# Performance work log

Measured on AMD Instinct MI355X. Metric: run time of the kernel, lower is better.

## Reference

```python
import jax, jax.numpy as jnp
import numpy as np
import math

SEQ = 45000
FEAT = 30
DEPTH, HEADS, DK, MLP, C = 4, 4, 32, 512, 32
MAXSEQ = 512


def pos_embed_table():
    # Enformer-style basis functions over distances [-SEQ+1, SEQ-1]
    d = jnp.arange(-SEQ + 1, SEQ, dtype=jnp.float32)
    a = jnp.abs(d)[:, None]
    nb = FEAT // 6  # basis per class (exponential / central-mask / gamma)
    # exponential decay
    hl = 2.0 ** jnp.linspace(3.0, math.log(SEQ) / math.log(2.0), nb)
    e1 = jnp.exp(-math.log(2.0) / hl[None, :] * a)
    # central mask
    cw = 2.0 ** jnp.arange(1, nb + 1, dtype=jnp.float32) - 1.0
    e2 = (cw[None, :] > a).astype(jnp.float32)
    # gamma pdf
    stddev = SEQ / (2 * nb)
    start_mean = SEQ / nb
    mean = jnp.linspace(start_mean, float(SEQ), nb)
    conc = (mean / stddev) ** 2
    rate = mean / stddev ** 2
    logp = jax.scipy.special.xlogy(conc - 1.0, a) - rate * a
    logz = jax.scipy.special.gammaln(conc) - conc * jnp.log(rate)
    p = jnp.exp(logp - logz) + 1e-8
    e3 = p / jnp.max(p)
    e = jnp.concatenate([e1, e2, e3], axis=-1)
    return jnp.concatenate([e, jnp.sign(d)[:, None] * e], axis=-1)  # [2*SEQ-1, FEAT]


def layernorm(x, g, b, eps=1e-5):
    mu = jnp.mean(x, axis=-1, keepdims=True)
    var = jnp.var(x, axis=-1, keepdims=True)
    return (x - mu) * jax.lax.rsqrt(var + eps) * g + b


def setup_inputs() -> dict:
    key = jax.random.key(0)
    ks = jax.random.split(key, 16)
    B, L = 2, SEQ
    HD = HEADS * DK
    s = 0.02
    return {
        "x_skip": jax.random.normal(ks[0], (B, C, L), jnp.float32),
        "attention": jax.random.uniform(ks[1], (B, 3, L), jnp.float32),
        "ln1_g": jnp.ones((DEPTH, C), jnp.float32),
        "ln1_b": jnp.zeros((DEPTH, C), jnp.float32),
        "Wq": jax.random.normal(ks[2], (DEPTH, C, HD), jnp.float32) * s,
        "Wk": jax.random.normal(ks[3], (DEPTH, C, HD), jnp.float32) * s,
        "Wv": jax.random.normal(ks[4], (DEPTH, C, HD), jnp.float32) * s,
        "Wrel": jax.random.normal(ks[5], (DEPTH, FEAT, HD), jnp.float32) * s,
        "rcb": jax.random.normal(ks[6], (DEPTH, HEADS, DK), jnp.float32),
        "rpb": jax.random.normal(ks[7], (DEPTH, HEADS, DK), jnp.float32),
        "Wo": jax.random.normal(ks[8], (DEPTH, HD, C), jnp.float32) * s,
        "bo": jnp.zeros((DEPTH, C), jnp.float32),
        "ln2_g": jnp.ones((DEPTH, C), jnp.float32),
        "ln2_b": jnp.zeros((DEPTH, C), jnp.float32),
        "W1": jax.random.normal(ks[9], (DEPTH, C, MLP), jnp.float32) * s,
        "b1": jnp.zeros((DEPTH, MLP), jnp.float32),
        "W2": jax.random.normal(ks[10], (DEPTH, MLP, C), jnp.float32) * s,
        "b2": jnp.zeros((DEPTH, C), jnp.float32),
    }


def reference(x_skip, attention, ln1_g, ln1_b, Wq, Wk, Wv, Wrel, rcb, rpb, Wo, bo, ln2_g, ln2_b, W1, b1, W2, b2):
    B, Cc, L = x_skip.shape
    half = MAXSEQ // 2
    x_emb = jnp.swapaxes(x_skip, 1, 2)  # [B, L, C]
    # top splice sites by acceptor / donor score
    acc = jnp.argsort(-attention[:, 1, :], axis=1)[:, :half]
    don = jnp.argsort(-attention[:, 2, :], axis=1)[:, :half]
    idx = jnp.sort(jnp.concatenate([acc, don], axis=1), axis=1)  # [B, n]
    n = idx.shape[1]
    diff = idx[:, :, None] - idx[:, None, :] + SEQ - 1  # [B, n, n]
    positions = pos_embed_table()[diff]  # [B, n, n, FEAT]
    emb = jnp.take_along_axis(x_emb, idx[:, :, None], axis=1)  # [B, n, C]
    scale = DK ** -0.5
    for l in range(DEPTH):
        h = layernorm(emb, ln1_g[l], ln1_b[l])
        q = (h @ Wq[l]).reshape(B, n, HEADS, DK).transpose(0, 2, 1, 3) * scale
        k = (h @ Wk[l]).reshape(B, n, HEADS, DK).transpose(0, 2, 1, 3)
        v = (h @ Wv[l]).reshape(B, n, HEADS, DK).transpose(0, 2, 1, 3)
        content = jnp.einsum('bhid,bhjd->bhij', q + rcb[l][None, :, None, :], k)
        rel_k = (positions @ Wrel[l]).reshape(B, n, n, HEADS, DK)  # b i j h d
        rel = jnp.einsum('bhid,bijhd->bhij', q + rpb[l][None, :, None, :], rel_k)
        attn_w = jax.nn.softmax(content + rel, axis=-1)
        o = jnp.einsum('bhij,bhjd->bhid', attn_w, v)
        o = o.transpose(0, 2, 1, 3).reshape(B, n, HEADS * DK)
        emb = emb + o @ Wo[l] + bo[l]
        h2 = layernorm(emb, ln2_g[l], ln2_b[l])
        emb = emb + jax.nn.gelu(h2 @ W1[l] + b1[l], approximate=False) @ W2[l] + b2[l]
    out = jnp.zeros_like(x_emb).at[jnp.arange(B)[:, None], idx].set(emb)
    return jnp.swapaxes(out, 1, 2)  # [B, C, L]
```

## Files before the change

kernel.cpp:

```cpp
#include <hip/hip_runtime.h>
#include <math.h>

#define SEQL   45000
#define NBAT   2
#define CCH    32
#define NSEL   512
#define NHEAD  4
#define DKD    32
#define HDD    128
#define MLPD   512
#define CDCAP  2048
#define TKB    32
#define ETB    176

__device__ __forceinline__ unsigned short f2bf(float x) {
  unsigned u = __float_as_uint(x);
  u = (u + 0x7fffu + ((u >> 16) & 1u)) >> 16;
  return (unsigned short)u;
}
#define BFL(u) __uint_as_float((u) << 16)
#define BFH(u) __uint_as_float((u) & 0xffff0000u)

__global__ __launch_bounds__(256) void prep_kernel(const float* __restrict__ att,
                                                   unsigned char* __restrict__ E16,
                                                   int* __restrict__ hist,
                                                   float* __restrict__ out) {
  {
    int nthr = gridDim.x * 256;
    int gt = blockIdx.x * 256 + threadIdx.x;
    float4 z4 = make_float4(0.f, 0.f, 0.f, 0.f);
    float4* o4 = (float4*)out;
    for (int i = gt; i < NBAT * CCH * SEQL / 4; i += nthr) o4[i] = z4;
  }
  if (blockIdx.x < ETB) {
    int a = blockIdx.x * 256 + threadIdx.x;
    if (a >= SEQL) return;
    float ad = (float)a;
    float outv[16];
    float log2S = log2f((float)SEQL);
    #pragma unroll
    for (int k = 0; k < 5; ++k) {
      float hl = exp2f(3.0f + (float)k * (log2S - 3.0f) * 0.25f);
      outv[k] = exp2f(-ad / hl);
    }
    const int cw[5] = {1, 3, 7, 15, 31};
    #pragma unroll
    for (int k = 0; k < 5; ++k) outv[5 + k] = (a < cw[k]) ? 1.0f : 0.0f;
    float pmax = 0.0f;
    float pk[5];
    #pragma unroll
    for (int k = 0; k < 5; ++k) {
      float mean = 9000.0f * (float)(k + 1);
      float sd = 4500.0f;
      float cc = (mean / sd) * (mean / sd);
      float rr = mean / (sd * sd);
      float logz = lgammaf(cc) - cc * logf(rr);
      float pp;
      if (a == 0) pp = 1e-8f;
      else pp = expf((cc - 1.0f) * logf(ad) - rr * ad - logz) + 1e-8f;
      pk[k] = pp;
      float mstar = (cc - 1.0f) / rr;
      float m0 = floorf(mstar), m1 = m0 + 1.0f;
      if (m1 > (float)(SEQL - 1)) m1 = (float)(SEQL - 1);
      float p0 = expf((cc - 1.0f) * logf(m0) - rr * m0 - logz) + 1e-8f;
      float p1 = expf((cc - 1.0f) * logf(m1) - rr * m1 - logz) + 1e-8f;
      pmax = fmaxf(pmax, fmaxf(p0, p1));
    }
    #pragma unroll
    for (int k = 0; k < 5; ++k) outv[10 + k] = pk[k] / pmax;
    outv[15] = 0.0f;
    unsigned by[16];
    #pragma unroll
    for (int k = 0; k < 15; ++k)
      by[k] = (unsigned)(fminf(fmaxf(outv[k], 0.f), 1.f) * 255.f + 0.5f);
    by[15] = 0u;
    unsigned pw[8];
    #pragma unroll
    for (int k = 0; k < 8; ++k)
      pw[k] = (unsigned)f2bf((float)by[2 * k]) |
              ((unsigned)f2bf((float)by[2 * k + 1]) << 16);
    uint4 o0 = make_uint4(pw[0], pw[1], pw[2], pw[3]);
    uint4 o1 = make_uint4(pw[4], pw[5], pw[6], pw[7]);
    uint4* dst = (uint4*)(E16 + (size_t)a * 32);
    dst[0] = o0;
    dst[1] = o1;
  } else {
    int bid = blockIdx.x - ETB;
    int ch4 = bid / TKB;
    int blk = bid % TKB;
    int b = ch4 >> 1, ch = ch4 & 1;
    const float* row = att + ((size_t)b * 3 + 1 + ch) * SEQL;
    int* h = hist + (size_t)ch4 * 65536;
    int per = (SEQL + TKB - 1) / TKB;
    int lo = blk * per;
    int hi = lo + per; if (hi > SEQL) hi = SEQL;
    for (int i = lo + threadIdx.x; i < hi; i += 256)
      atomicAdd(&h[__float_as_uint(row[i]) >> 16], 1);
  }
}

__global__ __launch_bounds__(256) void topk_collect_kernel(
    const float* __restrict__ att, const int* __restrict__ hist,
    unsigned long long* __restrict__ cand, int* __restrict__ cnt) {
  __shared__ int s_scan[256];
  __shared__ int s_aux[2];
  int tid = threadIdx.x;
  int ch4 = blockIdx.x / TKB;
  int blk = blockIdx.x % TKB;
  const int* h = hist + (size_t)ch4 * 65536;
  {
    int base = tid * 256;
    int sum = 0;
    for (int i = 0; i < 64; ++i) {
      int4 v = ((const int4*)(h + base))[i];
      sum += v.x + v.y + v.z + v.w;
    }
    s_scan[tid] = sum;
  }
  __syncthreads();
  for (int d = 1; d < 256; d <<= 1) {
    int v = s_scan[tid] + ((tid + d < 256) ? s_scan[tid + d] : 0);
    __syncthreads();
    s_scan[tid] = v;
    __syncthreads();
  }
  {
    int sufEx = (tid == 255) ? 0 : s_scan[tid + 1];
    if (s_scan[tid] >= 256 && sufEx < 256) { s_aux[0] = tid; s_aux[1] = 256 - sufEx; }
  }
  __syncthreads();
  int chunk = s_aux[0], want = s_aux[1];
  s_scan[tid] = h[chunk * 256 + tid];
  __syncthreads();
  for (int d = 1; d < 256; d <<= 1) {
    int v = s_scan[tid] + ((tid + d < 256) ? s_scan[tid + d] : 0);
    __syncthreads();
    s_scan[tid] = v;
    __syncthreads();
  }
  {
    int sufEx2 = (tid == 255) ? 0 : s_scan[tid + 1];
    if (s_scan[tid] >= want && sufEx2 < want) s_aux[0] = chunk * 256 + tid;
  }
  __syncthreads();
  unsigned T16 = (unsigned)s_aux[0];
  int b = ch4 >> 1, ch = ch4 & 1;
  const float* row = att + ((size_t)b * 3 + 1 + ch) * SEQL;
  int per = (SEQL + TKB - 1) / TKB;
  int lo = blk * per;
  int hi = lo + per; if (hi > SEQL) hi = SEQL;
  for (int i = lo + tid; i < hi; i += 256) {
    unsigned key = __float_as_uint(row[i]);
    if ((key >> 16) >= T16) {
      int p = atomicAdd(&cnt[ch4], 1);
      if (p < CDCAP)
        cand[(size_t)ch4 * CDCAP + p] =
            ((unsigned long long)key << 32) | (unsigned)(~(unsigned)i);
    }
  }
}

__global__ __launch_bounds__(1024) void topk_sort_kernel(
    const unsigned long long* __restrict__ cand, const int* __restrict__ cnt,
    unsigned* __restrict__ chsel) {
  __shared__ unsigned long long sc[CDCAP];
  int ch4 = blockIdx.x, t = threadIdx.x;
  int n = cnt[ch4]; if (n > CDCAP) n = CDCAP;
  int P = 256;
  while (P < n) P <<= 1;
  for (int i = t; i < P; i += 1024)
    sc[i] = (i < n) ? cand[(size_t)ch4 * CDCAP + i] : 0ull;
  __syncthreads();
  for (int k = 2; k <= P; k <<= 1) {
    for (int j = k >> 1; j > 0; j >>= 1) {
      for (int i = t; i < P; i += 1024) {
        int ixj = i ^ j;
        if (ixj > i) {
          unsigned long long va = sc[i], vb2 = sc[ixj];
          bool up = ((i & k) == 0);
          if ((va < vb2) == up) { sc[i] = vb2; sc[ixj] = va; }
        }
      }
      __syncthreads();
    }
  }
  if (t < 256)
    chsel[(size_t)ch4 * 256 + t] = ~(unsigned)(sc[t] & 0xFFFFFFFFull);
}

__global__ __launch_bounds__(512) void topk_merge_kernel(const unsigned* __restrict__ chsel,
                                                         int* __restrict__ idx) {
  __shared__ int m[512];
  int b = blockIdx.x, tid = threadIdx.x;
  m[tid] = (int)chsel[(size_t)b * 512 + tid];
  __syncthreads();
  for (int k = 2; k <= 512; k <<= 1) {
    for (int j = k >> 1; j > 0; j >>= 1) {
      int ixj = tid ^ j;
      if (ixj > tid) {
        int va = m[tid], vb2 = m[ixj];
        bool up = ((tid & k) == 0);
        if ((va > vb2) == up) { m[tid] = vb2; m[ixj] = va; }
      }
      __syncthreads();
    }
  }
  idx[b * 512 + tid] = m[tid];
}

__global__ __launch_bounds__(128) void gqkv0_kernel(
    const float* __restrict__ x, const int* __restrict__ idx,
    const float* __restrict__ ln_g, const float* __restrict__ ln_b,
    const float* __restrict__ Wq, const float* __restrict__ Wk,
    const float* __restrict__ Wv, const float* __restrict__ Wrel,
    const float* __restrict__ rcb, const float* __restrict__ rpb,
    float* __restrict__ emb, float* __restrict__ qc,
    unsigned short* __restrict__ kbT, unsigned short* __restrict__ vT,
    float* __restrict__ wb) {
  __shared__ float qs[128];
  const int l = 0;
  int hd = threadIdx.x;
  int hh = hd >> 5, d = hd & 31;
  int row = blockIdx.x;
  int b = row >> 9, ii = row & 511;
  int li = idx[b * NSEL + ii];
  float h[32];
  float mu = 0.f;
  #pragma unroll
  for (int c = 0; c < 32; ++c) {
    h[c] = x[((size_t)b * CCH + c) * SEQL + li];
    mu += h[c];
  }
  if (hd < 32) emb[(size_t)row * CCH + hd] = h[hd];
  mu *= (1.0f / 32.0f);
  float var = 0.f;
  #pragma unroll
  for (int c = 0; c < 32; ++c) { float dd0 = h[c] - mu; var += dd0 * dd0; }
  var *= (1.0f / 32.0f);
  float rstd = rsqrtf(var + 1e-5f);
  const float* g = ln_g + l * CCH;
  const float* bb = ln_b + l * CCH;
  #pragma unroll
  for (int c = 0; c < 32; ++c) h[c] = (h[c] - mu) * rstd * g[c] + bb[c];
  const float* wq = Wq + (size_t)l * CCH * HDD + hd;
  const float* wk = Wk + (size_t)l * CCH * HDD + hd;
  const float* wv = Wv + (size_t)l * CCH * HDD + hd;
  float q = 0.f, kk = 0.f, vv = 0.f;
  #pragma unroll
  for (int c = 0; c < 32; ++c) {
    q += h[c] * wq[c * HDD];
    kk += h[c] * wk[c * HDD];
    vv += h[c] * wv[c * HDD];
  }
  q *= 0.17677669529663687f;
  qs[hd] = q;
  qc[(size_t)row * HDD + hd] = q + rcb[(l * NHEAD + hh) * DKD + d];
  size_t tpos = ((size_t)(b * 4 + hh) * 4 + (d >> 3)) * 4096 + (size_t)ii * 8 + (d & 7);
  kbT[tpos] = f2bf(kk);
  vT[tpos]  = f2bf(vv);
  __syncthreads();
  if (hd < 120) {
    int h2 = hd / 30, f = hd % 30;
    const float* wr = Wrel + ((size_t)l * 30 + f) * HDD + h2 * DKD;
    const float* rp = rpb + (l * NHEAD + h2) * DKD;
    const float* qsh = qs + h2 * DKD;
    float acc = 0.f;
    #pragma unroll
    for (int dd = 0; dd < 32; ++dd) acc += (qsh[dd] + rp[dd]) * wr[dd];
    wb[((size_t)row * NHEAD + h2) * 32 + f] = acc;
  }
}

__global__ __launch_bounds__(256, 4) void layer_kernel(
    const float* __restrict__ qc, const unsigned short* __restrict__ kbT,
    const unsigned short* __restrict__ vT, const float* __restrict__ wbuf,
    const unsigned char* __restrict__ E16, const int* __restrict__ idx,
    const float* __restrict__ Wo, const float* __restrict__ bo,
    const float* __restrict__ ln2_g, const float* __restrict__ ln2_b,
    const float* __restrict__ W1, const float* __restrict__ b1,
    const float* __restrict__ W2, const float* __restrict__ b2,
    const float* __restrict__ ln1_g, const float* __restrict__ ln1_b,
    const float* __restrict__ Wq, const float* __restrict__ Wk,
    const float* __restrict__ Wv, const float* __restrict__ Wrel,
    const float* __restrict__ rcb, const float* __restrict__ rpb,
    float* __restrict__ emb, float* __restrict__ qcN,
    unsigned short* __restrict__ kbTN, unsigned short* __restrict__ vTN,
    float* __restrict__ wbN, float* __restrict__ out, int layer) {
  __shared__ unsigned esb[8 * 512];
  __shared__ float obs[128];
  __shared__ float part[8][32];
  __shared__ float res[32];
  __shared__ float hln[32];
  __shared__ float fin[32];
  __shared__ float a1s[MLPD];
  __shared__ float qs[128];
  int bid = blockIdx.x;
  int b = bid >> 9;
  int i = bid & 511;
  int tid = threadIdx.x;
  int pos = idx[b * NSEL + i];
  #pragma unroll
  for (int rep = 0; rep < 2; ++rep) {
    int j = tid + rep * 256;
    int dj = pos - idx[b * NSEL + j];
    int a = dj < 0 ? -dj : dj;
    const uint4* eg = (const uint4*)(E16 + (size_t)a * 32);
    uint4 e0 = eg[0];
    uint4 e1 = eg[1];
    unsigned sc = dj > 0 ? 0x3F80u : (dj < 0 ? 0xBF80u : 0u);
    e1.w |= (sc << 16);
    uint4* ed = (uint4*)(esb + j * 8);
    ed[0] = e0;
    ed[1] = e1;
  }
  __syncthreads();
  {
    int h = tid >> 6, ln = tid & 63;
    const float* qrow = qc + (size_t)(b * NSEL + i) * HDD + h * DKD;
    float q[32];
    #pragma unroll
    for (int d4 = 0; d4 < 8; ++d4) {
      float4 qv = *(const float4*)(qrow + d4 * 4);
      q[d4 * 4 + 0] = qv.x; q[d4 * 4 + 1] = qv.y;
      q[d4 * 4 + 2] = qv.z; q[d4 * 4 + 3] = qv.w;
    }
    const float* wrow = wbuf + ((size_t)(b * NSEL + i) * NHEAD + h) * 32;
    float w0[15], w1[15];
    #pragma unroll
    for (int f = 0; f < 15; ++f) {
      w0[f] = wrow[f] * (1.0f / 255.0f);
      w1[f] = wrow[15 + f] * (1.0f / 255.0f);
    }
    const uint4* kb4 = (const uint4*)kbT + (size_t)(b * 4 + h) * 4 * 512;
    const uint4* vb4 = (const uint4*)vT + (size_t)(b * 4 + h) * 4 * 512;
    float lg[8];
    #pragma unroll
    for (int u = 0; u < 8; ++u) {
      int j = u * 64 + ln;
      float cacc = 0.f;
      #pragma unroll
      for (int dp = 0; dp < 4; ++dp) {
        uint4 kv = kb4[dp * 512 + j];
        cacc += q[dp * 8 + 0] * BFL(kv.x) + q[dp * 8 + 1] * BFH(kv.x)
              + q[dp * 8 + 2] * BFL(kv.y) + q[dp * 8 + 3] * BFH(kv.y)
              + q[dp * 8 + 4] * BFL(kv.z) + q[dp * 8 + 5] * BFH(kv.z)
              + q[dp * 8 + 6] * BFL(kv.w) + q[dp * 8 + 7] * BFH(kv.w);
      }
      const uint4* ej = (const uint4*)(esb + j * 8);
      uint4 a0 = ej[0];
      uint4 a1 = ej[1];
      float r0, r1;
      r0  = BFL(a0.x) * w0[0]  + BFH(a0.x) * w0[1];
      r1  = BFL(a0.x) * w1[0]  + BFH(a0.x) * w1[1];
      r0 += BFL(a0.y) * w0[2]  + BFH(a0.y) * w0[3];
      r1 += BFL(a0.y) * w1[2]  + BFH(a0.y) * w1[3];
      r0 += BFL(a0.z) * w0[4]  + BFH(a0.z) * w0[5];
      r1 += BFL(a0.z) * w1[4]  + BFH(a0.z) * w1[5];
      r0 += BFL(a0.w) * w0[6]  + BFH(a0.w) * w0[7];
      r1 += BFL(a0.w) * w1[6]  + BFH(a0.w) * w1[7];
      r0 += BFL(a1.x) * w0[8]  + BFH(a1.x) * w0[9];
      r1 += BFL(a1.x) * w1[8]  + BFH(a1.x) * w1[9];
      r0 += BFL(a1.y) * w0[10] + BFH(a1.y) * w0[11];
      r1 += BFL(a1.y) * w1[10] + BFH(a1.y) * w1[11];
      r0 += BFL(a1.z) * w0[12] + BFH(a1.z) * w0[13];
      r1 += BFL(a1.z) * w1[12] + BFH(a1.z) * w1[13];
      r0 += BFL(a1.w) * w0[14];
      r1 += BFL(a1.w) * w1[14];
      lg[u] = cacc + r0 + BFH(a1.w) * r1;
    }
    float m = lg[0];
    #pragma unroll
    for (int u = 1; u < 8; ++u) m = fmaxf(m, lg[u]);
    #pragma unroll
    for (int s = 1; s < 64; s <<= 1) m = fmaxf(m, __shfl_xor(m, s));
    float ssum = 0.f;
    #pragma unroll
    for (int u = 0; u < 8; ++u) { lg[u] = __expf(lg[u] - m); ssum += lg[u]; }
    #pragma unroll
    for (int s = 1; s < 64; s <<= 1) ssum += __shfl_xor(ssum, s);
    float invs = 1.0f / ssum;
    #pragma unroll
    for (int dp = 0; dp < 4; ++dp) {
      float acc[8] = {0.f, 0.f, 0.f, 0.f, 0.f, 0.f, 0.f, 0.f};
      #pragma unroll
      for (int u = 0; u < 8; ++u) {
        uint4 vv = vb4[dp * 512 + u * 64 + ln];
        float p = lg[u];
        acc[0] += p * BFL(vv.x); acc[1] += p * BFH(vv.x);
        acc[2] += p * BFL(vv.y); acc[3] += p * BFH(vv.y);
        acc[4] += p * BFL(vv.z); acc[5] += p * BFH(vv.z);
        acc[6] += p * BFL(vv.w); acc[7] += p * BFH(vv.w);
      }
      #pragma unroll
      for (int s = 1; s < 8; s <<= 1) {
        #pragma unroll
        for (int t = 0; t < 8; ++t) acc[t] += __shfl_xor(acc[t], s);
      }
      int sel = ln & 7;
      float y = acc[0];
      #pragma unroll
      for (int t = 1; t < 8; ++t) y = (sel == t) ? acc[t] : y;
      #pragma unroll
      for (int s = 8; s < 64; s <<= 1) y += __shfl_xor(y, s);
      if (ln < 8) obs[h * DKD + dp * 8 + ln] = y * invs;
    }
  }
  __syncthreads();
  int c = tid & 31, seg = tid >> 5;
  {
    const float* wo = Wo + (size_t)layer * HDD * CCH + c;
    float pacc = 0.f;
    #pragma unroll
    for (int k = 0; k < 16; ++k) {
      int kk = seg * 16 + k;
      pacc += obs[kk] * wo[kk * CCH];
    }
    part[seg][c] = pacc;
  }
  __syncthreads();
  if (tid < 32) {
    float s = bo[layer * CCH + tid] + emb[(size_t)bid * CCH + tid];
    #pragma unroll
    for (int sg = 0; sg < 8; ++sg) s += part[sg][tid];
    res[tid] = s;
  }
  __syncthreads();
  if (tid < 32) {
    float mu = 0.f, s2 = 0.f;
    #pragma unroll
    for (int c2 = 0; c2 < 32; ++c2) { float v = res[c2]; mu += v; s2 += v * v; }
    mu *= (1.0f / 32.0f);
    float var = s2 * (1.0f / 32.0f) - mu * mu;
    float rstd = rsqrtf(var + 1e-5f);
    hln[tid] = (res[tid] - mu) * rstd * ln2_g[layer * CCH + tid] + ln2_b[layer * CCH + tid];
  }
  __syncthreads();
  {
    const float* w1 = W1 + (size_t)layer * CCH * MLPD;
    float accA = b1[layer * MLPD + tid];
    float accB = b1[layer * MLPD + tid + 256];
    for (int c2 = 0; c2 < 32; ++c2) {
      float hv = hln[c2];
      accA += hv * w1[c2 * MLPD + tid];
      accB += hv * w1[c2 * MLPD + tid + 256];
    }
    a1s[tid]       = 0.5f * accA * (1.0f + erff(accA * 0.70710678118654752f));
    a1s[tid + 256] = 0.5f * accB * (1.0f + erff(accB * 0.70710678118654752f));
  }
  __syncthreads();
  {
    const float* w2 = W2 + (size_t)layer * MLPD * CCH;
    float acc2 = 0.f;
    #pragma unroll 4
    for (int mi = 0; mi < 64; ++mi) {
      int m = seg * 64 + mi;
      acc2 += a1s[m] * w2[m * CCH + c];
    }
    __syncthreads();
    part[seg][c] = acc2;
  }
  __syncthreads();
  if (tid < 32) {
    float s = b2[layer * CCH + tid] + res[tid];
    #pragma unroll
    for (int sg = 0; sg < 8; ++sg) s += part[sg][tid];
    fin[tid] = s;
    if (layer < 3) emb[(size_t)bid * CCH + tid] = s;
  }
  __syncthreads();
  if (layer == 3) {
    if (tid < 32) out[((size_t)b * CCH + tid) * SEQL + pos] = fin[tid];
    return;
  }
  const int l1 = layer + 1;
  bool act = tid < 128;
  int hd = tid & 127;
  int hh2 = hd >> 5, dd2 = hd & 31;
  if (act) {
    float hx[32];
    float mu = 0.f;
    #pragma unroll
    for (int c2 = 0; c2 < 32; ++c2) { hx[c2] = fin[c2]; mu += hx[c2]; }
    mu *= (1.0f / 32.0f);
    float var = 0.f;
    #pragma unroll
    for (int c2 = 0; c2 < 32; ++c2) { float dd = hx[c2] - mu; var += dd * dd; }
    var *= (1.0f / 32.0f);
    float rstd = rsqrtf(var + 1e-5f);
    const float* g = ln1_g + l1 * CCH;
    const float* bb = ln1_b + l1 * CCH;
    #pragma unroll
    for (int c2 = 0; c2 < 32; ++c2) hx[c2] = (hx[c2] - mu) * rstd * g[c2] + bb[c2];
    const float* wq = Wq + (size_t)l1 * CCH * HDD + hd;
    const float* wk = Wk + (size_t)l1 * CCH * HDD + hd;
    const float* wv = Wv + (size_t)l1 * CCH * HDD + hd;
    float q = 0.f, kk = 0.f, vv = 0.f;
    #pragma unroll
    for (int c2 = 0; c2 < 32; ++c2) {
      q += hx[c2] * wq[c2 * HDD];
      kk += hx[c2] * wk[c2 * HDD];
      vv += hx[c2] * wv[c2 * HDD];
    }
    q *= 0.17677669529663687f;
    qs[hd] = q;
    qcN[(size_t)bid * HDD + hd] = q + rcb[(l1 * NHEAD + hh2) * DKD + dd2];
    size_t tpos = ((size_t)(b * 4 + hh2) * 4 + (dd2 >> 3)) * 4096 + (size_t)i * 8 + (dd2 & 7);
    kbTN[tpos] = f2bf(kk);
    vTN[tpos]  = f2bf(vv);
  }
  __syncthreads();
  if (act && hd < 120) {
    int h2 = hd / 30, f = hd % 30;
    const float* rp = rpb + (l1 * NHEAD + h2) * DKD;
    const float* wr = Wrel + ((size_t)l1 * 30 + f) * HDD + h2 * DKD;
    const float* qsh = qs + h2 * DKD;
    float acc = 0.f;
    #pragma unroll
    for (int dd = 0; dd < 32; ++dd) acc += (qsh[dd] + rp[dd]) * wr[dd];
    wbN[((size_t)bid * NHEAD + h2) * 32 + f] = acc;
  }
}

extern "C" void kernel_launch(void* const* d_in, const int* in_sizes, int n_in,
                              void* d_out, int out_size, void* d_ws, size_t ws_size,
                              hipStream_t stream) {
  (void)in_sizes; (void)n_in; (void)ws_size; (void)out_size;
  const float* x_skip    = (const float*)d_in[0];
  const float* attention = (const float*)d_in[1];
  const float* ln1_g = (const float*)d_in[2];
  const float* ln1_b = (const float*)d_in[3];
  const float* Wq    = (const float*)d_in[4];
  const float* Wk    = (const float*)d_in[5];
  const float* Wv    = (const float*)d_in[6];
  const float* Wrel  = (const float*)d_in[7];
  const float* rcb   = (const float*)d_in[8];
  const float* rpb   = (const float*)d_in[9];
  const float* Wo    = (const float*)d_in[10];
  const float* bo    = (const float*)d_in[11];
  const float* ln2_g = (const float*)d_in[12];
  const float* ln2_b = (const float*)d_in[13];
  const float* W1    = (const float*)d_in[14];
  const float* b1    = (const float*)d_in[15];
  const float* W2    = (const float*)d_in[16];
  const float* b2    = (const float*)d_in[17];
  float* out = (float*)d_out;
  char* ws = (char*)d_ws;

  unsigned char* E16 = (unsigned char*)(ws + 0);
  int*      idx   = (int*)(ws + 1441792);
  float*    emb   = (float*)(ws + 1445888);
  float*    qcA   = (float*)(ws + 1576960);
  unsigned short* kbTA = (unsigned short*)(ws + 2101248);
  unsigned short* vTA  = (unsigned short*)(ws + 2363392);
  float*    wbA   = (float*)(ws + 2625536);
  unsigned short* kbTB = (unsigned short*)(ws + 3149824);
  unsigned short* vTB  = (unsigned short*)(ws + 3411968);
  int*      hist  = (int*)(ws + 3674112);
  int*      cnt   = (int*)(ws + 4722688);
  unsigned long long* cand = (unsigned long long*)(ws + 4722720);
  unsigned* chsel = (unsigned*)(ws + 4788256);
  float*    qcB   = (float*)(ws + 4792352);
  float*    wbB   = (float*)(ws + 5316640);

  hipMemsetAsync(ws + 3674112, 0, 1048576 + 32, stream);
  prep_kernel<<<ETB + 4 * TKB, 256, 0, stream>>>(attention, E16, hist, out);
  topk_collect_kernel<<<4 * TKB, 256, 0, stream>>>(attention, hist, cand, cnt);
  topk_sort_kernel<<<4, 1024, 0, stream>>>(cand, cnt, chsel);
  topk_merge_kernel<<<2, 512, 0, stream>>>(chsel, idx);
  gqkv0_kernel<<<1024, 128, 0, stream>>>(x_skip, idx, ln1_g, ln1_b, Wq, Wk, Wv,
                                         Wrel, rcb, rpb, emb, qcA, kbTA, vTA, wbA);
  for (int l = 0; l < 4; ++l) {
    const float* qcI = (l & 1) ? qcB : qcA;
    const unsigned short* kbI = (l & 1) ? kbTB : kbTA;
    const unsigned short* vI  = (l & 1) ? vTB : vTA;
    const float* wbI = (l & 1) ? wbB : wbA;
    float* qcO = (l & 1) ? qcA : qcB;
    unsigned short* kbO = (l & 1) ? kbTA : kbTB;
    unsigned short* vO  = (l & 1) ? vTA : vTB;
    float* wbO = (l & 1) ? wbA : wbB;
    layer_kernel<<<1024, 256, 0, stream>>>(qcI, kbI, vI, wbI, E16, idx,
                                           Wo, bo, ln2_g, ln2_b, W1, b1, W2, b2,
                                           ln1_g, ln1_b, Wq, Wk, Wv, Wrel, rcb,
                                           rpb, emb, qcO, kbO, vO, wbO, out, l);
  }
}
```

Measured before the change: 298.1 us.

## Double layer kernel block to 512 threads, split attention keys across two waves per head

The per-query layer kernel now launches 512 threads instead of 256. Each head's 512 keys are split between two wavefronts, and the partial softmax max and sum are merged through shared memory before rescaling the V accumulations. The Wo, MLP and W2 reductions are re-split over 16 segments to match. This roughly halves the serial work per thread, at the cost of extra syncs, a cross-wave softmax merge, and higher register and occupancy pressure from the 512,8 launch bounds.

```diff
diff --git a/kernel.cpp b/kernel.cpp
--- a/kernel.cpp
+++ b/kernel.cpp
@@ -271,7 +271,7 @@
   }
 }
 
-__global__ __launch_bounds__(256, 4) void layer_kernel(
+__global__ __launch_bounds__(512, 8) void layer_kernel(
     const float* __restrict__ qc, const unsigned short* __restrict__ kbT,
     const unsigned short* __restrict__ vT, const float* __restrict__ wbuf,
     const unsigned char* __restrict__ E16, const int* __restrict__ idx,
@@ -287,21 +287,22 @@
     unsigned short* __restrict__ kbTN, unsigned short* __restrict__ vTN,
     float* __restrict__ wbN, float* __restrict__ out, int layer) {
   __shared__ unsigned esb[8 * 512];
+  __shared__ float obsp[8][32];
   __shared__ float obs[128];
-  __shared__ float part[8][32];
+  __shared__ float part[16][32];
   __shared__ float res[32];
   __shared__ float hln[32];
   __shared__ float fin[32];
   __shared__ float a1s[MLPD];
   __shared__ float qs[128];
+  __shared__ float smx[8], ssm[8];
   int bid = blockIdx.x;
   int b = bid >> 9;
   int i = bid & 511;
   int tid = threadIdx.x;
   int pos = idx[b * NSEL + i];
-  #pragma unroll
-  for (int rep = 0; rep < 2; ++rep) {
-    int j = tid + rep * 256;
+  {
+    int j = tid;
     int dj = pos - idx[b * NSEL + j];
     int a = dj < 0 ? -dj : dj;
     const uint4* eg = (const uint4*)(E16 + (size_t)a * 32);
@@ -314,8 +315,12 @@
     ed[1] = e1;
   }
   __syncthreads();
-  {
-    int h = tid >> 6, ln = tid & 63;
+  int wv = tid >> 6;
+  int h = wv >> 1, hf = wv & 1, ln = tid & 63;
+  float lg[4];
+  const uint4* kb4 = (const uint4*)kbT + (size_t)(b * 4 + h) * 4 * 512;
+  const uint4* vb4 = (const uint4*)vT + (size_t)(b * 4 + h) * 4 * 512;
+  {
     const float* qrow = qc + (size_t)(b * NSEL + i) * HDD + h * DKD;
     float q[32];
     #pragma unroll
@@ -331,12 +336,9 @@
       w0[f] = wrow[f] * (1.0f / 255.0f);
       w1[f] = wrow[15 + f] * (1.0f / 255.0f);
     }
-    const uint4* kb4 = (const uint4*)kbT + (size_t)(b * 4 + h) * 4 * 512;
-    const uint4* vb4 = (const uint4*)vT + (size_t)(b * 4 + h) * 4 * 512;
-    float lg[8];
-    #pragma unroll
-    for (int u = 0; u < 8; ++u) {
-      int j = u * 64 + ln;
+    #pragma unroll
+    for (int u = 0; u < 4; ++u) {
+      int j = hf * 256 + u * 64 + ln;
       float cacc = 0.f;
       #pragma unroll
       for (int dp = 0; dp < 4; ++dp) {
@@ -370,49 +372,61 @@
     }
     float m = lg[0];
     #pragma unroll
-    for (int u = 1; u < 8; ++u) m = fmaxf(m, lg[u]);
+    for (int u = 1; u < 4; ++u) m = fmaxf(m, lg[u]);
     #pragma unroll
     for (int s = 1; s < 64; s <<= 1) m = fmaxf(m, __shfl_xor(m, s));
     float ssum = 0.f;
     #pragma unroll
-    for (int u = 0; u < 8; ++u) { lg[u] = __expf(lg[u] - m); ssum += lg[u]; }
+    for (int u = 0; u < 4; ++u) { lg[u] = __expf(lg[u] - m); ssum += lg[u]; }
     #pragma unroll
     for (int s = 1; s < 64; s <<= 1) ssum += __shfl_xor(ssum, s);
-    float invs = 1.0f / ssum;
-    #pragma unroll
-    for (int dp = 0; dp < 4; ++dp) {
-      float acc[8] = {0.f, 0.f, 0.f, 0.f, 0.f, 0.f, 0.f, 0.f};
+    if (ln == 0) { smx[wv] = m; ssm[wv] = ssum; }
+  }
+  __syncthreads();
+  float factor;
+  {
+    float m0 = smx[h * 2], m1 = smx[h * 2 + 1];
+    float mm = fmaxf(m0, m1);
+    float stot = ssm[h * 2] * __expf(m0 - mm) + ssm[h * 2 + 1] * __expf(m1 - mm);
+    float mw = hf ? m1 : m0;
+    factor = __expf(mw - mm) / stot;
+  }
+  #pragma unroll
+  for (int dp = 0; dp < 4; ++dp) {
+    float acc[8] = {0.f, 0.f, 0.f, 0.f, 0.f, 0.f, 0.f, 0.f};
+    #pragma unroll
+    for (int u = 0; u < 4; ++u) {
+      uint4 vvv = vb4[dp * 512 + hf * 256 + u * 64 + ln];
+      float p = lg[u];
+      acc[0] += p * BFL(vvv.x); acc[1] += p * BFH(vvv.x);
+      acc[2] += p * BFL(vvv.y); acc[3] += p * BFH(vvv.y);
+      acc[4] += p * BFL(vvv.z); acc[5] += p * BFH(vvv.z);
+      acc[6] += p * BFL(vvv.w); acc[7] += p * BFH(vvv.w);
+    }
+    #pragma unroll
+    for (int s = 1; s < 8; s <<= 1) {
       #pragma unroll
-      for (int u = 0; u < 8; ++u) {
-        uint4 vv = vb4[dp * 512 + u * 64 + ln];
-        float p = lg[u];
-        acc[0] += p * BFL(vv.x); acc[1] += p * BFH(vv.x);
-        acc[2] += p * BFL(vv.y); acc[3] += p * BFH(vv.y);
-        acc[4] += p * BFL(vv.z); acc[5] += p * BFH(vv.z);
-        acc[6] += p * BFL(vv.w); acc[7] += p * BFH(vv.w);
-      }
-      #pragma unroll
-      for (int s = 1; s < 8; s <<= 1) {
-        #pragma unroll
-        for (int t = 0; t < 8; ++t) acc[t] += __shfl_xor(acc[t], s);
-      }
-      int sel = ln & 7;
-      float y = acc[0];
-      #pragma unroll
-      for (int t = 1; t < 8; ++t) y = (sel == t) ? acc[t] : y;
-      #pragma unroll
-      for (int s = 8; s < 64; s <<= 1) y += __shfl_xor(y, s);
-      if (ln < 8) obs[h * DKD + dp * 8 + ln] = y * invs;
-    }
-  }
+      for (int t = 0; t < 8; ++t) acc[t] += __shfl_xor(acc[t], s);
+    }
+    int sel = ln & 7;
+    float y = acc[0];
+    #pragma unroll
+    for (int t = 1; t < 8; ++t) y = (sel == t) ? acc[t] : y;
+    #pragma unroll
+    for (int s = 8; s < 64; s <<= 1) y += __shfl_xor(y, s);
+    if (ln < 8) obsp[wv][dp * 8 + ln] = y * factor;
+  }
+  __syncthreads();
+  if (tid < 128)
+    obs[tid] = obsp[(tid >> 5) * 2][tid & 31] + obsp[(tid >> 5) * 2 + 1][tid & 31];
   __syncthreads();
   int c = tid & 31, seg = tid >> 5;
   {
     const float* wo = Wo + (size_t)layer * HDD * CCH + c;
     float pacc = 0.f;
     #pragma unroll
-    for (int k = 0; k < 16; ++k) {
-      int kk = seg * 16 + k;
+    for (int k = 0; k < 8; ++k) {
+      int kk = seg * 8 + k;
       pacc += obs[kk] * wo[kk * CCH];
     }
     part[seg][c] = pacc;
@@ -421,8 +435,9 @@
   if (tid < 32) {
     float s = bo[layer * CCH + tid] + emb[(size_t)bid * CCH + tid];
     #pragma unroll
-    for (int sg = 0; sg < 8; ++sg) s += part[sg][tid];
+    for (int sg = 0; sg < 16; ++sg) s += part[sg][tid];
     res[tid] = s;
+    float mu = 0.f, s2 = 0.f;
   }
   __syncthreads();
   if (tid < 32) {
@@ -438,22 +453,16 @@
   {
     const float* w1 = W1 + (size_t)layer * CCH * MLPD;
     float accA = b1[layer * MLPD + tid];
-    float accB = b1[layer * MLPD + tid + 256];
-    for (int c2 = 0; c2 < 32; ++c2) {
-      float hv = hln[c2];
-      accA += hv * w1[c2 * MLPD + tid];
-      accB += hv * w1[c2 * MLPD + tid + 256];
-    }
-    a1s[tid]       = 0.5f * accA * (1.0f + erff(accA * 0.70710678118654752f));
-    a1s[tid + 256] = 0.5f * accB * (1.0f + erff(accB * 0.70710678118654752f));
+    for (int c2 = 0; c2 < 32; ++c2) accA += hln[c2] * w1[c2 * MLPD + tid];
+    a1s[tid] = 0.5f * accA * (1.0f + erff(accA * 0.70710678118654752f));
   }
   __syncthreads();
   {
     const float* w2 = W2 + (size_t)layer * MLPD * CCH;
     float acc2 = 0.f;
     #pragma unroll 4
-    for (int mi = 0; mi < 64; ++mi) {
-      int m = seg * 64 + mi;
+    for (int mi = 0; mi < 32; ++mi) {
+      int m = seg * 32 + mi;
       acc2 += a1s[m] * w2[m * CCH + c];
     }
     __syncthreads();
@@ -463,7 +472,7 @@
   if (tid < 32) {
     float s = b2[layer * CCH + tid] + res[tid];
     #pragma unroll
-    for (int sg = 0; sg < 8; ++sg) s += part[sg][tid];
+    for (int sg = 0; sg < 16; ++sg) s += part[sg][tid];
     fin[tid] = s;
     if (layer < 3) emb[(size_t)bid * CCH + tid] = s;
   }
@@ -494,19 +503,19 @@
     const float* wq = Wq + (size_t)l1 * CCH * HDD + hd;
     const float* wk = Wk + (size_t)l1 * CCH * HDD + hd;
     const float* wv = Wv + (size_t)l1 * CCH * HDD + hd;
-    float q = 0.f, kk = 0.f, vv = 0.f;
+    float q = 0.f, kk = 0.f, vvv = 0.f;
     #pragma unroll
     for (int c2 = 0; c2 < 32; ++c2) {
       q += hx[c2] * wq[c2 * HDD];
       kk += hx[c2] * wk[c2 * HDD];
-      vv += hx[c2] * wv[c2 * HDD];
+      vvv += hx[c2] * wv[c2 * HDD];
     }
     q *= 0.17677669529663687f;
     qs[hd] = q;
     qcN[(size_t)bid * HDD + hd] = q + rcb[(l1 * NHEAD + hh2) * DKD + dd2];
     size_t tpos = ((size_t)(b * 4 + hh2) * 4 + (dd2 >> 3)) * 4096 + (size_t)i * 8 + (dd2 & 7);
     kbTN[tpos] = f2bf(kk);
-    vTN[tpos]  = f2bf(vv);
+    vTN[tpos]  = f2bf(vvv);
   }
   __syncthreads();
   if (act && hd < 120) {
@@ -578,7 +587,7 @@
     unsigned short* kbO = (l & 1) ? kbTA : kbTB;
     unsigned short* vO  = (l & 1) ? vTA : vTB;
     float* wbO = (l & 1) ? wbA : wbB;
-    layer_kernel<<<1024, 256, 0, stream>>>(qcI, kbI, vI, wbI, E16, idx,
+    layer_kernel<<<1024, 512, 0, stream>>>(qcI, kbI, vI, wbI, E16, idx,
                                            Wo, bo, ln2_g, ln2_b, W1, b1, W2, b2,
                                            ln1_g, ln1_b, Wq, Wk, Wv, Wrel, rcb,
                                            rpb, emb, qcO, kbO, vO, wbO, out, l);
```

Result: slower. 530.3 us (+77.9%).
